# Optimization experiments

Measured on AMD Instinct MI355X. Metric: run time of the kernel, lower is better.

## Reference

```python
import jax, jax.numpy as jnp
import numpy as np

N, C, T, V = 64, 256, 64, 25

def setup_inputs() -> dict:
    key = jax.random.key(0)
    ks = jax.random.split(key, 11)
    inp = {
        't': jax.random.uniform(ks[0], (1,), dtype=jnp.float32),
        'x': jax.random.normal(ks[1], (N, C, T, V), dtype=jnp.float32),
        'A': jax.random.normal(ks[2], (V, V), dtype=jnp.float32) * 0.2,
    }
    for i in range(4):
        inp[f'w{i+1}'] = jax.random.normal(ks[3 + 2 * i], (C, C), dtype=jnp.float32) * (1.0 / np.sqrt(C))
        inp[f'b{i+1}'] = jax.random.normal(ks[4 + 2 * i], (C,), dtype=jnp.float32) * 0.02
    return inp


def _block(res, A, w, b):
    # graph diffusion over joint dim: A[v,u] @ x[n,c,t,u]
    y = jnp.einsum('vu,nctu->nctv', A, res)
    # 1x1 conv == pointwise channel GEMM
    y = jnp.einsum('oc,nctv->notv', w, y) + b[None, :, None, None]
    return jax.nn.relu(y + res)


def reference(t, x, A, w1, b1, w2, b2, w3, b3, w4, b4):
    # t is unused by the ODE function body (autonomous dynamics)
    res = _block(x, A, w1, b1)
    res = _block(res, A, w2, b2)
    res = _block(res, A, w3, b3)
    res = _block(res, A, w4, b4)
    return res
```

## Files before the change

kernel.cpp:

```cpp
#include <hip/hip_runtime.h>
#include <math.h>

#define NN 64
#define CC 256
#define TT 64
#define VV 25

typedef __bf16 bf16;
typedef __attribute__((ext_vector_type(8)))  __bf16 bf16x8;
typedef __attribute__((ext_vector_type(4)))  __bf16 bf16x4;
typedef __attribute__((ext_vector_type(16))) float  f32x16;

#define RS 40
#define YS 264

#define OFF_SRES  0
#define OFF_SYT   20480
#define OFF_SAB   34208
#define OFF_SBIAS 36256
#define SMEM_BYTES 40352

__global__ void convert_w(const float* __restrict__ w1, const float* __restrict__ w2,
                          const float* __restrict__ w3, const float* __restrict__ w4,
                          bf16* __restrict__ wp) {
    const int gid = blockIdx.x * 256 + threadIdx.x;
    const int e8  = gid * 8;
    const int blk = e8 >> 16;
    const int off = e8 & 65535;
    const int row = off >> 8;
    const int col = off & 255;
    const float* src = (blk == 0) ? w1 : (blk == 1) ? w2 : (blk == 2) ? w3 : w4;
    const float4 f0 = *(const float4*)(src + off);
    const float4 f1 = *(const float4*)(src + off + 4);
    bf16x8 o;
    o[0] = (bf16)f0.x; o[1] = (bf16)f0.y; o[2] = (bf16)f0.z; o[3] = (bf16)f0.w;
    o[4] = (bf16)f1.x; o[5] = (bf16)f1.y; o[6] = (bf16)f1.z; o[7] = (bf16)f1.w;
    const int wv = row >> 6, pair = (row >> 5) & 1, l31 = row & 31;
    const int k = col >> 4, lh = (col >> 3) & 1;
    wp += (((size_t)(blk * 4 + wv) * 16 + k) * 1024) + pair * 512 + (lh * 32 + l31) * 8;
    *(bf16x8*)wp = o;
}

#define MFMA(A, B, C) __builtin_amdgcn_mfma_f32_32x32x16_bf16(A, B, C, 0, 0, 0)

__global__ __launch_bounds__(256, 4) void ode_mfma(
    const float* __restrict__ x, const float* __restrict__ Amat,
    const bf16* __restrict__ wp,
    const float* __restrict__ b1, const float* __restrict__ b2,
    const float* __restrict__ b3, const float* __restrict__ b4,
    float* __restrict__ out)
{
    __shared__ __attribute__((aligned(16))) char smem[SMEM_BYTES];
    bf16*  sres  = (bf16*)(smem + OFF_SRES);
    bf16*  syT   = (bf16*)(smem + OFF_SYT);
    bf16*  sAb   = (bf16*)(smem + OFF_SAB);
    float* sbias = (float*)(smem + OFF_SBIAS);

    const int t    = blockIdx.x;
    const int n    = blockIdx.y;
    const int tid  = threadIdx.x;
    const int wave = tid >> 6;
    const int lane = tid & 63;
    const int lh   = lane >> 5;
    const int l31  = lane & 31;

    sbias[0 * CC + tid] = b1[tid];
    sbias[1 * CC + tid] = b2[tid];
    sbias[2 * CC + tid] = b3[tid];
    sbias[3 * CC + tid] = b4[tid];

    for (int i = tid; i < 32 * 32; i += 256) {
        const int v = i >> 5, u = i & 31;
        sAb[i] = (v < VV && u < VV) ? (bf16)Amat[v * VV + u] : (bf16)0.f;
    }

    {
        const float* xb = x + ((size_t)n * CC * TT + t) * VV;
        for (int i = tid; i < CC * VV; i += 256) {
            const int c = i / VV;
            const int v = i - c * VV;
            sres[c * RS + v] = (bf16)xb[(size_t)c * TT * VV + v];
        }
        #pragma unroll
        for (int u = VV; u < 32; ++u) sres[tid * RS + u] = (bf16)0.f;
    }
    __syncthreads();

    const bf16x8 bfA0 = *(const bf16x8*)&sAb[l31 * 32 + lh * 8];
    const bf16x8 bfA1 = *(const bf16x8*)&sAb[l31 * 32 + 16 + lh * 8];

    for (int blk = 0; blk < 4; ++blk) {
        #pragma unroll
        for (int i = 0; i < 2; ++i) {
            const int ct = wave * 2 + i;
            const bf16x8 af0 = *(const bf16x8*)&sres[(ct * 32 + l31) * RS + lh * 8];
            const bf16x8 af1 = *(const bf16x8*)&sres[(ct * 32 + l31) * RS + 16 + lh * 8];
            f32x16 d = {};
            d = MFMA(af0, bfA0, d);
            d = MFMA(af1, bfA1, d);
            if (l31 < VV) {
                #pragma unroll
                for (int g = 0; g < 4; ++g) {
                    bf16x4 p;
                    p[0] = (bf16)d[4 * g];     p[1] = (bf16)d[4 * g + 1];
                    p[2] = (bf16)d[4 * g + 2]; p[3] = (bf16)d[4 * g + 3];
                    *(bf16x4*)&syT[l31 * YS + ct * 32 + 8 * g + 4 * lh] = p;
                }
            }
        }
        __syncthreads();

        const bf16* wbase = wp + ((size_t)(blk * 4 + wave) * 16) * 1024 + lane * 8;
        const int o0 = wave * 64;

        f32x16 acc0 = {}, acc1 = {};
        #pragma unroll 4
        for (int k = 0; k < 16; ++k) {
            const bf16x8 y0 = *(const bf16x8*)&syT[l31 * YS + k * 16 + lh * 8];
            const bf16x8 a0 = *(const bf16x8*)(wbase + k * 1024);
            const bf16x8 a1 = *(const bf16x8*)(wbase + k * 1024 + 512);
            acc0 = MFMA(a0, y0, acc0);
            acc1 = MFMA(a1, y0, acc1);
        }

        const int v = l31;
        #define EPILOGUE(ACC, OT)                                                   \
            _Pragma("unroll")                                                       \
            for (int g = 0; g < 4; ++g) {                                           \
                const int ob = o0 + (OT) * 32 + 8 * g + 4 * lh;                     \
                const float4 bq = *(const float4*)&sbias[blk * CC + ob];            \
                _Pragma("unroll")                                                   \
                for (int r = 0; r < 4; ++r) {                                       \
                    const int o = ob + r;                                           \
                    float val = ACC[4 * g + r] + ((const float*)&bq)[r]             \
                              + (float)sres[o * RS + v];                            \
                    val = fmaxf(val, 0.f);                                          \
                    if (v < VV) {                                                   \
                        if (blk < 3) sres[o * RS + v] = (bf16)val;                  \
                        else out[(((size_t)n * CC + o) * TT + t) * VV + v] = val;   \
                    }                                                               \
                }                                                                   \
            }
        EPILOGUE(acc0, 0)
        EPILOGUE(acc1, 1)
        #undef EPILOGUE
        __syncthreads();
    }
}

extern "C" void kernel_launch(void* const* d_in, const int* in_sizes, int n_in,
                              void* d_out, int out_size, void* d_ws, size_t ws_size,
                              hipStream_t stream) {
    const float* x  = (const float*)d_in[1];
    const float* A  = (const float*)d_in[2];
    const float* w1 = (const float*)d_in[3];
    const float* b1 = (const float*)d_in[4];
    const float* w2 = (const float*)d_in[5];
    const float* b2 = (const float*)d_in[6];
    const float* w3 = (const float*)d_in[7];
    const float* b3 = (const float*)d_in[8];
    const float* w4 = (const float*)d_in[9];
    const float* b4 = (const float*)d_in[10];
    float* out = (float*)d_out;
    bf16* wp = (bf16*)d_ws;

    convert_w<<<128, 256, 0, stream>>>(w1, w2, w3, w4, wp);
    dim3 grid(TT, NN);
    ode_mfma<<<grid, 256, 0, stream>>>(x, A, wp, b1, b2, b3, b4, out);
}
```

Measured before the change: 380.0 us.

## Process eight timesteps per block with register-resident weights and residuals

Each block now covers 8 consecutive timesteps for one sample, using 512 threads (8 waves) instead of 4 waves for a single timestep. Each wave keeps its 32-row weight slice in registers for the whole block, so one weight load is reused across 8 timesteps, and the residual state also lives in packed registers. The syT buffer is double-buffered, which removes one barrier per step. The cost is much higher register pressure, only 512 blocks, and uncoalesced strided global loads and stores for x and out.

```diff
diff --git a/kernel.cpp b/kernel.cpp
--- a/kernel.cpp
+++ b/kernel.cpp
@@ -7,6 +7,7 @@
 #define VV 25
 
 typedef __bf16 bf16;
+typedef unsigned int u32;
 typedef __attribute__((ext_vector_type(8)))  __bf16 bf16x8;
 typedef __attribute__((ext_vector_type(4)))  __bf16 bf16x4;
 typedef __attribute__((ext_vector_type(16))) float  f32x16;
@@ -14,11 +15,20 @@
 #define RS 40
 #define YS 264
 
-#define OFF_SRES  0
-#define OFF_SYT   20480
-#define OFF_SAB   34208
-#define OFF_SBIAS 36256
-#define SMEM_BYTES 40352
+static __device__ __forceinline__ u32 pk2(float a, float b) {
+    unsigned short ua = __builtin_bit_cast(unsigned short, (bf16)a);
+    unsigned short ub = __builtin_bit_cast(unsigned short, (bf16)b);
+    return (u32)ua | ((u32)ub << 16);
+}
+static __device__ __forceinline__ float uplo(u32 w) {
+    return (float)__builtin_bit_cast(bf16, (unsigned short)(w & 0xffffu));
+}
+static __device__ __forceinline__ float uphi(u32 w) {
+    return (float)__builtin_bit_cast(bf16, (unsigned short)(w >> 16));
+}
+static __device__ __forceinline__ bf16 us2bf(unsigned short u) {
+    return __builtin_bit_cast(bf16, u);
+}
 
 __global__ void convert_w(const float* __restrict__ w1, const float* __restrict__ w2,
                           const float* __restrict__ w3, const float* __restrict__ w4,
@@ -35,116 +45,121 @@
     bf16x8 o;
     o[0] = (bf16)f0.x; o[1] = (bf16)f0.y; o[2] = (bf16)f0.z; o[3] = (bf16)f0.w;
     o[4] = (bf16)f1.x; o[5] = (bf16)f1.y; o[6] = (bf16)f1.z; o[7] = (bf16)f1.w;
-    const int wv = row >> 6, pair = (row >> 5) & 1, l31 = row & 31;
-    const int k = col >> 4, lh = (col >> 3) & 1;
-    wp += (((size_t)(blk * 4 + wv) * 16 + k) * 1024) + pair * 512 + (lh * 32 + l31) * 8;
-    *(bf16x8*)wp = o;
+    const int ot = row >> 5, l31r = row & 31;
+    const int k = col >> 4, lhc = (col >> 3) & 1;
+    *(bf16x8*)(wp + ((size_t)(((blk * 8 + ot) * 16 + k) * 64) + lhc * 32 + l31r) * 8) = o;
 }
 
 #define MFMA(A, B, C) __builtin_amdgcn_mfma_f32_32x32x16_bf16(A, B, C, 0, 0, 0)
 
-__global__ __launch_bounds__(256, 4) void ode_mfma(
+__global__ __launch_bounds__(512, 2) void ode_fused(
     const float* __restrict__ x, const float* __restrict__ Amat,
     const bf16* __restrict__ wp,
     const float* __restrict__ b1, const float* __restrict__ b2,
     const float* __restrict__ b3, const float* __restrict__ b4,
     float* __restrict__ out)
 {
-    __shared__ __attribute__((aligned(16))) char smem[SMEM_BYTES];
-    bf16*  sres  = (bf16*)(smem + OFF_SRES);
-    bf16*  syT   = (bf16*)(smem + OFF_SYT);
-    bf16*  sAb   = (bf16*)(smem + OFF_SAB);
-    float* sbias = (float*)(smem + OFF_SBIAS);
+    __shared__ bf16  syT[2][32][YS];
+    __shared__ bf16  scm[CC][RS];
+    __shared__ float sbias[4][CC];
+    __shared__ bf16  sAb[32][32];
 
-    const int t    = blockIdx.x;
-    const int n    = blockIdx.y;
     const int tid  = threadIdx.x;
-    const int wave = tid >> 6;
+    const int wv   = tid >> 6;
     const int lane = tid & 63;
     const int lh   = lane >> 5;
     const int l31  = lane & 31;
+    const int n    = blockIdx.x >> 3;
+    const int t0   = (blockIdx.x & 7) * 8;
 
-    sbias[0 * CC + tid] = b1[tid];
-    sbias[1 * CC + tid] = b2[tid];
-    sbias[2 * CC + tid] = b3[tid];
-    sbias[3 * CC + tid] = b4[tid];
-
-    for (int i = tid; i < 32 * 32; i += 256) {
+    if (tid < 256) { sbias[0][tid] = b1[tid]; sbias[1][tid] = b2[tid]; }
+    else { const int c = tid - 256; sbias[2][c] = b3[c]; sbias[3][c] = b4[c]; }
+    for (int i = tid; i < 1024; i += 512) {
         const int v = i >> 5, u = i & 31;
-        sAb[i] = (v < VV && u < VV) ? (bf16)Amat[v * VV + u] : (bf16)0.f;
-    }
-
-    {
-        const float* xb = x + ((size_t)n * CC * TT + t) * VV;
-        for (int i = tid; i < CC * VV; i += 256) {
-            const int c = i / VV;
-            const int v = i - c * VV;
-            sres[c * RS + v] = (bf16)xb[(size_t)c * TT * VV + v];
-        }
-        #pragma unroll
-        for (int u = VV; u < 32; ++u) sres[tid * RS + u] = (bf16)0.f;
+        sAb[v][u] = (v < VV && u < VV) ? (bf16)Amat[v * VV + u] : (bf16)0.f;
     }
     __syncthreads();
 
-    const bf16x8 bfA0 = *(const bf16x8*)&sAb[l31 * 32 + lh * 8];
-    const bf16x8 bfA1 = *(const bf16x8*)&sAb[l31 * 32 + 16 + lh * 8];
+    const bf16x8 AB0 = *(const bf16x8*)&sAb[l31][lh * 8];
+    const bf16x8 AB1 = *(const bf16x8*)&sAb[l31][16 + lh * 8];
+
+    u32 rp[8][8];
+    {
+        const int vq = (l31 < VV) ? l31 : VV - 1;
+        const float* xb = x + ((size_t)n * CC * TT + t0) * VV + vq;
+        #pragma unroll
+        for (int s = 0; s < 8; ++s) {
+            #pragma unroll
+            for (int m = 0; m < 8; ++m) {
+                const int o0 = 32 * wv + 4 * lh + 2 * (m & 1) + 8 * (m >> 1);
+                const float f0 = xb[((size_t)o0 * TT + s) * VV];
+                const float f1 = xb[((size_t)(o0 + 1) * TT + s) * VV];
+                rp[s][m] = pk2(f0, f1);
+            }
+        }
+    }
 
     for (int blk = 0; blk < 4; ++blk) {
+        bf16x8 wf[16];
+        const bf16* wpb = wp + ((size_t)((blk * 8 + wv) * 16) * 64 + lane) * 8;
         #pragma unroll
-        for (int i = 0; i < 2; ++i) {
-            const int ct = wave * 2 + i;
-            const bf16x8 af0 = *(const bf16x8*)&sres[(ct * 32 + l31) * RS + lh * 8];
-            const bf16x8 af1 = *(const bf16x8*)&sres[(ct * 32 + l31) * RS + 16 + lh * 8];
+        for (int k = 0; k < 16; ++k) wf[k] = *(const bf16x8*)(wpb + (size_t)k * 512);
+
+        float bq[16];
+        #pragma unroll
+        for (int r = 0; r < 16; ++r)
+            bq[r] = sbias[blk][32 * wv + (r & 3) + 8 * (r >> 2) + 4 * lh];
+
+        #pragma unroll
+        for (int s = 0; s < 8; ++s) {
+            const int buf = s & 1;
+            #pragma unroll
+            for (int m = 0; m < 8; ++m) {
+                const u32 w = rp[s][m];
+                const int c0 = 32 * wv + 4 * lh + 2 * (m & 1) + 8 * (m >> 1);
+                scm[c0][l31]     = us2bf((unsigned short)(w & 0xffffu));
+                scm[c0 + 1][l31] = us2bf((unsigned short)(w >> 16));
+            }
+            const bf16x8 af0 = *(const bf16x8*)&scm[32 * wv + l31][lh * 8];
+            const bf16x8 af1 = *(const bf16x8*)&scm[32 * wv + l31][16 + lh * 8];
             f32x16 d = {};
-            d = MFMA(af0, bfA0, d);
-            d = MFMA(af1, bfA1, d);
+            d = MFMA(af0, AB0, d);
+            d = MFMA(af1, AB1, d);
             if (l31 < VV) {
                 #pragma unroll
                 for (int g = 0; g < 4; ++g) {
                     bf16x4 p;
                     p[0] = (bf16)d[4 * g];     p[1] = (bf16)d[4 * g + 1];
                     p[2] = (bf16)d[4 * g + 2]; p[3] = (bf16)d[4 * g + 3];
-                    *(bf16x4*)&syT[l31 * YS + ct * 32 + 8 * g + 4 * lh] = p;
+                    *(bf16x4*)&syT[buf][l31][32 * wv + 8 * g + 4 * lh] = p;
+                }
+            }
+            __syncthreads();
+
+            f32x16 acc0 = {}, acc1 = {};
+            #pragma unroll
+            for (int k = 0; k < 16; k += 2) {
+                const bf16x8 y0 = *(const bf16x8*)&syT[buf][l31][k * 16 + lh * 8];
+                const bf16x8 y1 = *(const bf16x8*)&syT[buf][l31][(k + 1) * 16 + lh * 8];
+                acc0 = MFMA(wf[k], y0, acc0);
+                acc1 = MFMA(wf[k + 1], y1, acc1);
+            }
+
+            #pragma unroll
+            for (int m = 0; m < 8; ++m) {
+                const int r0 = 2 * m;
+                const int o0 = 32 * wv + 4 * lh + 2 * (m & 1) + 8 * (m >> 1);
+                float v0 = acc0[r0] + acc1[r0] + bq[r0] + uplo(rp[s][m]);
+                float v1 = acc0[r0 + 1] + acc1[r0 + 1] + bq[r0 + 1] + uphi(rp[s][m]);
+                v0 = fmaxf(v0, 0.f);
+                v1 = fmaxf(v1, 0.f);
+                rp[s][m] = pk2(v0, v1);
+                if (blk == 3 && l31 < VV) {
+                    out[(((size_t)n * CC + o0) * TT + t0 + s) * VV + l31]     = v0;
+                    out[(((size_t)n * CC + o0 + 1) * TT + t0 + s) * VV + l31] = v1;
                 }
             }
         }
-        __syncthreads();
-
-        const bf16* wbase = wp + ((size_t)(blk * 4 + wave) * 16) * 1024 + lane * 8;
-        const int o0 = wave * 64;
-
-        f32x16 acc0 = {}, acc1 = {};
-        #pragma unroll 4
-        for (int k = 0; k < 16; ++k) {
-            const bf16x8 y0 = *(const bf16x8*)&syT[l31 * YS + k * 16 + lh * 8];
-            const bf16x8 a0 = *(const bf16x8*)(wbase + k * 1024);
-            const bf16x8 a1 = *(const bf16x8*)(wbase + k * 1024 + 512);
-            acc0 = MFMA(a0, y0, acc0);
-            acc1 = MFMA(a1, y0, acc1);
-        }
-
-        const int v = l31;
-        #define EPILOGUE(ACC, OT)                                                   \
-            _Pragma("unroll")                                                       \
-            for (int g = 0; g < 4; ++g) {                                           \
-                const int ob = o0 + (OT) * 32 + 8 * g + 4 * lh;                     \
-                const float4 bq = *(const float4*)&sbias[blk * CC + ob];            \
-                _Pragma("unroll")                                                   \
-                for (int r = 0; r < 4; ++r) {                                       \
-                    const int o = ob + r;                                           \
-                    float val = ACC[4 * g + r] + ((const float*)&bq)[r]             \
-                              + (float)sres[o * RS + v];                            \
-                    val = fmaxf(val, 0.f);                                          \
-                    if (v < VV) {                                                   \
-                        if (blk < 3) sres[o * RS + v] = (bf16)val;                  \
-                        else out[(((size_t)n * CC + o) * TT + t) * VV + v] = val;   \
-                    }                                                               \
-                }                                                                   \
-            }
-        EPILOGUE(acc0, 0)
-        EPILOGUE(acc1, 1)
-        #undef EPILOGUE
-        __syncthreads();
     }
 }
 
@@ -165,6 +180,5 @@
     bf16* wp = (bf16*)d_ws;
 
     convert_w<<<128, 256, 0, stream>>>(w1, w2, w3, w4, wp);
-    dim3 grid(TT, NN);
-    ode_mfma<<<grid, 256, 0, stream>>>(x, A, wp, b1, b2, b3, b4, out);
+    ode_fused<<<512, 512, 0, stream>>>(x, A, wp, b1, b2, b3, b4, out);
 }
```

New measurement: 427.1 us. +12.4%, slower.
